# Kernel tuning notes

Measured on AMD Instinct MI355X. Metric: run time of the kernel, lower is better.

Reference implementation:

```python
import jax, jax.numpy as jnp
import numpy as np

N = 65536   # batch
G = 7       # grid
C = 2       # classes (cats vs dogs)
A = 3       # anchors


def _bce(p, t):
    return -(t * jnp.log(p) + (1.0 - t) * jnp.log(1.0 - p))


def _iou(a, b):
    # a, b: [..., 4] boxes in (cx, cy, w, h) format
    ax1, ay1 = a[..., 0] - a[..., 2] / 2, a[..., 1] - a[..., 3] / 2
    ax2, ay2 = a[..., 0] + a[..., 2] / 2, a[..., 1] + a[..., 3] / 2
    bx1, by1 = b[..., 0] - b[..., 2] / 2, b[..., 1] - b[..., 3] / 2
    bx2, by2 = b[..., 0] + b[..., 2] / 2, b[..., 1] + b[..., 3] / 2
    iw = jnp.clip(jnp.minimum(ax2, bx2) - jnp.maximum(ax1, bx1), 0.0)
    ih = jnp.clip(jnp.minimum(ay2, by2) - jnp.maximum(ay1, by1), 0.0)
    inter = iw * ih
    union = (ax2 - ax1) * (ay2 - ay1) + (bx2 - bx1) * (by2 - by1) - inter
    return inter / (union + 1e-9)


def setup_inputs():
    key = jax.random.key(0)
    k1, k2, k3, k4 = jax.random.split(key, 4)
    # probabilities / box params must lie strictly in (0,1) for BCE and log()
    bbox_ = jax.random.uniform(k1, (N, 15, G, G), dtype=jnp.float32, minval=0.01, maxval=0.99)
    bbox = jax.random.uniform(k2, (N, 5, G, G), dtype=jnp.float32, minval=0.01, maxval=0.99)
    cls_ = jax.random.normal(k3, (N, C), dtype=jnp.float32)
    cls = jax.random.randint(k4, (N,), 1, 3).astype(jnp.int64)  # labels in {1,2}
    return {"bbox_": bbox_, "cls_": cls_, "bbox": bbox, "cls": cls}


def reference(bbox_, cls_, bbox, cls):
    n = bbox.shape[0]
    bidx = jnp.arange(n)

    # classification: CrossEntropyLoss (mean) with labels cls-1
    logp = jax.nn.log_softmax(cls_, axis=-1)
    ce = -jnp.mean(jnp.take_along_axis(logp, (cls - 1)[:, None], axis=1))

    # argmax cell of GT objectness map per sample
    probs = bbox[:, 0]                       # [N,7,7]
    m = jnp.argmax(probs.reshape(n, -1), axis=1)
    i, j = m // G, m % G                     # [N], [N]

    cell_gt = bbox[bidx, :, i, j]            # [N,5]
    cell_pr = bbox_[bidx, :, i, j].reshape(n, A, 5)  # [N,3,5]

    jf = j.astype(bbox.dtype)
    if_ = i.astype(bbox.dtype)

    # target box in global coords
    tgt = jnp.stack([(cell_gt[:, 1] + jf) / G, (cell_gt[:, 2] + if_) / G,
                     cell_gt[:, 3], cell_gt[:, 4]], axis=-1)          # [N,4]
    # anchor boxes in global coords
    anc = jnp.stack([(cell_pr[:, :, 1] + jf[:, None]) / G,
                     (cell_pr[:, :, 2] + if_[:, None]) / G,
                     cell_pr[:, :, 3], cell_pr[:, :, 4]], axis=-1)    # [N,3,4]

    best = jnp.argmax(_iou(anc, tgt[:, None, :]), axis=1)             # [N]

    # target objectness maps: best anchor channel gets GT prob map
    target_prob = jnp.zeros((n, A, G, G), dtype=bbox.dtype)
    target_prob = target_prob.at[bidx, best].set(probs)

    # coordinate BCE (sum) + size L1-of-logs (sum) at the matched cell/anchor
    best_box = cell_pr[bidx, best]           # [N,5]
    coord = jnp.sum(_bce(best_box[:, 1:3], cell_gt[:, 1:3]))
    size = jnp.sum(jnp.abs(jnp.log(best_box[:, 3:5]) - jnp.log(cell_gt[:, 3:5])))

    # per-anchor objectness BCE (mean over N*49 each)
    prob_loss = (jnp.mean(_bce(bbox_[:, 0], target_prob[:, 0]))
                 + jnp.mean(_bce(bbox_[:, 5], target_prob[:, 1]))
                 + jnp.mean(_bce(bbox_[:, 10], target_prob[:, 2])))

    return ce + coord + size + prob_loss
```

## Files before the change

### kernel.cpp

```cpp
#include <hip/hip_runtime.h>
#include <math.h>


static constexpr int GG  = 49;
static constexpr int PRD = 15 * GG;
static constexpr int GTD = 5  * GG;
static constexpr int GOF = 768;
static constexpr int LPW = 1024;

__global__ void zero_kernel(float* out) { if (threadIdx.x == 0) out[0] = 0.0f; }

__global__ __launch_bounds__(256) void loss_kernel(
    const float* __restrict__ pr_all,
    const float* __restrict__ cls_logits,
    const float* __restrict__ gt_all,
    const int*   __restrict__ cls_lbl,
    float* __restrict__ out, int N)
{
    const int lane  = threadIdx.x & 63;
    const int wslot = threadIdx.x >> 6;
    const int wid   = blockIdx.x * (blockDim.x >> 6) + wslot;
    const int nwaves = gridDim.x * (blockDim.x >> 6);
    const float invG   = 1.0f / 7.0f;
    const float invN   = 1.0f / (float)N;
    const float invN49 = 1.0f / ((float)N * 49.0f);

    __shared__ float L[4][LPW];
    float* __restrict__ Lw = L[wslot];

    float acc = 0.0f;

    for (int n = wid; n < N; n += nwaves) {
        const float* pr = pr_all + (size_t)n * PRD;
        const float* gt = gt_all + (size_t)n * GTD;

        const float x0 = __builtin_nontemporal_load(cls_logits + 2 * n);
        const float x1 = __builtin_nontemporal_load(cls_logits + 2 * n + 1);
        const int   cl = __builtin_nontemporal_load(cls_lbl + n);

        float p[12];
        #pragma unroll
        for (int k = 0; k < 12; ++k) {
            int d = lane + 64 * k;
            if (d > PRD - 1) d = PRD - 1;
            p[k] = __builtin_nontemporal_load(pr + d);
        }
        float g[4];
        #pragma unroll
        for (int k = 0; k < 4; ++k) {
            int d = lane + 64 * k;
            if (d > GTD - 1) d = GTD - 1;
            g[k] = __builtin_nontemporal_load(gt + d);
        }

        #pragma unroll
        for (int k = 0; k < 12; ++k) {
            int d = lane + 64 * k;
            if (d > PRD - 1) d = PRD - 1;
            Lw[d] = p[k];
        }
        #pragma unroll
        for (int k = 0; k < 4; ++k) {
            int d = lane + 64 * k;
            if (d > GTD - 1) d = GTD - 1;
            Lw[GOF + d] = g[k];
        }
        asm volatile("s_waitcnt lgkmcnt(0)" ::: "memory");

        const float t = (lane < GG) ? g[0] : -1.0f;
        float v = t;
        #pragma unroll
        for (int off = 32; off; off >>= 1) v = fmaxf(v, __shfl_xor(v, off));
        const unsigned long long eq = __ballot(t == v);
        const int m  = __ffsll(eq) - 1;
        const int mi = m / 7, mj = m - mi * 7;
        const float jf = (float)mj, if_ = (float)mi;

        const float g1v = Lw[GOF +  49 + m];
        const float g2v = Lw[GOF +  98 + m];
        const float g3v = Lw[GOF + 147 + m];
        const float g4v = Lw[GOF + 196 + m];

        const float tx  = (g1v + jf) * invG;
        const float ty  = (g2v + if_) * invG;
        const float tx1 = tx - g3v * 0.5f, tx2 = tx + g3v * 0.5f;
        const float ty1 = ty - g4v * 0.5f, ty2 = ty + g4v * 0.5f;
        const float tarea = (tx2 - tx1) * (ty2 - ty1);

        int best = 0; float bestIoU = -1.0f;
        float px = 0.f, py = 0.f, pw = 0.f, ph = 0.f;
        #pragma unroll
        for (int a = 0; a < 3; a++) {
            const float c1 = Lw[(5 * a + 1) * GG + m];
            const float c2 = Lw[(5 * a + 2) * GG + m];
            const float c3 = Lw[(5 * a + 3) * GG + m];
            const float c4 = Lw[(5 * a + 4) * GG + m];
            const float ax  = (c1 + jf) * invG;
            const float ay  = (c2 + if_) * invG;
            const float ax1 = ax - c3 * 0.5f, ax2 = ax + c3 * 0.5f;
            const float ay1 = ay - c4 * 0.5f, ay2 = ay + c4 * 0.5f;
            float iw = fminf(ax2, tx2) - fmaxf(ax1, tx1); iw = fmaxf(iw, 0.0f);
            float ih = fminf(ay2, ty2) - fmaxf(ay1, ty1); ih = fmaxf(ih, 0.0f);
            const float inter = iw * ih;
            const float uni   = (ax2 - ax1) * (ay2 - ay1) + tarea - inter;
            const float iou   = inter / (uni + 1e-9f);
            if (iou > bestIoU) { bestIoU = iou; best = a; px = c1; py = c2; pw = c3; ph = c4; }
        }

        float s = 0.0f;
        if (lane < GG) {
            const float p0 = p[0];
            const float p1 = Lw[5 * GG  + lane];
            const float p2 = Lw[10 * GG + lane];
            const float l0 = __logf(1.0f - p0);
            const float l1 = __logf(1.0f - p1);
            const float l2 = __logf(1.0f - p2);
            s = -(l0 + l1 + l2);
            const float pbv  = (best == 0) ? p0 : (best == 1) ? p1 : p2;
            const float l1pb = (best == 0) ? l0 : (best == 1) ? l1 : l2;
            s -= t * (__logf(pbv) - l1pb);
        }
        acc += s * invN49;

        const float s0  = (lane < 4) ? ((lane < 2) ? px : py)
                                     : ((lane < 6) ? pw : ph);
        const float s1  = (lane < 4) ? (1.0f - s0)
                                     : ((lane < 6) ? g3v : g4v);
        const float la  = (lane & 1) ? s1 : s0;
        const float Lv  = __logf(la);
        const float Lx  = __shfl_xor(Lv, 1);
        float contrib = 0.0f;
        if (lane < 4) {
            const float w = (lane < 2) ? ((lane & 1) ? 1.0f - g1v : g1v)
                                       : ((lane & 1) ? 1.0f - g2v : g2v);
            contrib = -w * Lv;
        } else if (lane == 4 || lane == 6) {
            contrib = fabsf(Lv - Lx);
        }
        acc += contrib;

        if (lane == 5) {
            const float mx  = fmaxf(x0, x1);
            const float lse = mx + __logf(1.0f + __expf(-fabsf(x0 - x1)));
            const float lp  = ((cl == 1) ? x0 : x1) - lse;
            acc -= lp * invN;
        }
    }

    #pragma unroll
    for (int off = 32; off; off >>= 1) acc += __shfl_xor(acc, off);
    __shared__ float wsum[4];
    if (lane == 0) wsum[wslot] = acc;
    __syncthreads();
    if (threadIdx.x == 0) {
        atomicAdd(out, wsum[0] + wsum[1] + wsum[2] + wsum[3]);
    }
}

extern "C" void kernel_launch(void* const* d_in, const int* in_sizes, int n_in,
                              void* d_out, int out_size, void* d_ws, size_t ws_size,
                              hipStream_t stream) {
    const float* bbox_p = (const float*)d_in[0];
    const float* cls_p  = (const float*)d_in[1];
    const float* bbox_g = (const float*)d_in[2];
    const int*   cls_l  = (const int*)d_in[3];
    float* out = (float*)d_out;
    const int N = in_sizes[3];

    hipLaunchKernelGGL(zero_kernel, dim3(1), dim3(64), 0, stream, out);
    hipLaunchKernelGGL(loss_kernel, dim3(2048), dim3(256), 0, stream,
                       bbox_p, cls_p, bbox_g, cls_l, out, N);
}
```

Before: 296.7 us.

## Replace LDS staging with register readlane and shuffle-based gathers

New measurement: 301.7 us. About the same (+1.7%).

```diff
diff --git a/kernel.cpp b/kernel.cpp
--- a/kernel.cpp
+++ b/kernel.cpp
@@ -5,10 +5,12 @@
 static constexpr int GG  = 49;
 static constexpr int PRD = 15 * GG;
 static constexpr int GTD = 5  * GG;
-static constexpr int GOF = 768;
-static constexpr int LPW = 1024;
 
 __global__ void zero_kernel(float* out) { if (threadIdx.x == 0) out[0] = 0.0f; }
+
+__device__ __forceinline__ float rdl(float x, int l) {
+    return __int_as_float(__builtin_amdgcn_readlane(__float_as_int(x), l & 63));
+}
 
 __global__ __launch_bounds__(256) void loss_kernel(
     const float* __restrict__ pr_all,
@@ -24,9 +26,6 @@
     const float invG   = 1.0f / 7.0f;
     const float invN   = 1.0f / (float)N;
     const float invN49 = 1.0f / ((float)N * 49.0f);
-
-    __shared__ float L[4][LPW];
-    float* __restrict__ Lw = L[wslot];
 
     float acc = 0.0f;
 
@@ -53,20 +52,6 @@
             g[k] = __builtin_nontemporal_load(gt + d);
         }
 
-        #pragma unroll
-        for (int k = 0; k < 12; ++k) {
-            int d = lane + 64 * k;
-            if (d > PRD - 1) d = PRD - 1;
-            Lw[d] = p[k];
-        }
-        #pragma unroll
-        for (int k = 0; k < 4; ++k) {
-            int d = lane + 64 * k;
-            if (d > GTD - 1) d = GTD - 1;
-            Lw[GOF + d] = g[k];
-        }
-        asm volatile("s_waitcnt lgkmcnt(0)" ::: "memory");
-
         const float t = (lane < GG) ? g[0] : -1.0f;
         float v = t;
         #pragma unroll
@@ -76,10 +61,11 @@
         const int mi = m / 7, mj = m - mi * 7;
         const float jf = (float)mj, if_ = (float)mi;
 
-        const float g1v = Lw[GOF +  49 + m];
-        const float g2v = Lw[GOF +  98 + m];
-        const float g3v = Lw[GOF + 147 + m];
-        const float g4v = Lw[GOF + 196 + m];
+        const int d1 = 49 + m, d2 = 98 + m, d3 = 147 + m, d4 = 196 + m;
+        const float g1v = (d1 < 64)  ? rdl(g[0], d1) : rdl(g[1], d1);
+        const float g2v = (d2 < 128) ? rdl(g[1], d2) : rdl(g[2], d2);
+        const float g3v = (d3 < 192) ? rdl(g[2], d3) : rdl(g[3], d3);
+        const float g4v = rdl(g[3], d4);
 
         const float tx  = (g1v + jf) * invG;
         const float ty  = (g2v + if_) * invG;
@@ -91,35 +77,49 @@
         float px = 0.f, py = 0.f, pw = 0.f, ph = 0.f;
         #pragma unroll
         for (int a = 0; a < 3; a++) {
-            const float c1 = Lw[(5 * a + 1) * GG + m];
-            const float c2 = Lw[(5 * a + 2) * GG + m];
-            const float c3 = Lw[(5 * a + 3) * GG + m];
-            const float c4 = Lw[(5 * a + 4) * GG + m];
-            const float ax  = (c1 + jf) * invG;
-            const float ay  = (c2 + if_) * invG;
-            const float ax1 = ax - c3 * 0.5f, ax2 = ax + c3 * 0.5f;
-            const float ay1 = ay - c4 * 0.5f, ay2 = ay + c4 * 0.5f;
+            float c[4];
+            #pragma unroll
+            for (int cc = 0; cc < 4; ++cc) {
+                const int S  = (5 * a + 1 + cc) * GG;
+                const int k0 = S >> 6;
+                const int k1 = (S + GG - 1) >> 6;
+                const int d  = S + m;
+                c[cc] = (k0 == k1) ? rdl(p[k0], d)
+                      : (((d >> 6) == k0) ? rdl(p[k0], d) : rdl(p[k1], d));
+            }
+            const float ax  = (c[0] + jf) * invG;
+            const float ay  = (c[1] + if_) * invG;
+            const float ax1 = ax - c[2] * 0.5f, ax2 = ax + c[2] * 0.5f;
+            const float ay1 = ay - c[3] * 0.5f, ay2 = ay + c[3] * 0.5f;
             float iw = fminf(ax2, tx2) - fmaxf(ax1, tx1); iw = fmaxf(iw, 0.0f);
             float ih = fminf(ay2, ty2) - fmaxf(ay1, ty1); ih = fmaxf(ih, 0.0f);
             const float inter = iw * ih;
             const float uni   = (ax2 - ax1) * (ay2 - ay1) + tarea - inter;
             const float iou   = inter / (uni + 1e-9f);
-            if (iou > bestIoU) { bestIoU = iou; best = a; px = c1; py = c2; pw = c3; ph = c4; }
+            if (iou > bestIoU) { bestIoU = iou; best = a;
+                                 px = c[0]; py = c[1]; pw = c[2]; ph = c[3]; }
         }
 
-        float s = 0.0f;
-        if (lane < GG) {
-            const float p0 = p[0];
-            const float p1 = Lw[5 * GG  + lane];
-            const float p2 = Lw[10 * GG + lane];
-            const float l0 = __logf(1.0f - p0);
-            const float l1 = __logf(1.0f - p1);
-            const float l2 = __logf(1.0f - p2);
-            s = -(l0 + l1 + l2);
-            const float pbv  = (best == 0) ? p0 : (best == 1) ? p1 : p2;
-            const float l1pb = (best == 0) ? l0 : (best == 1) ? l1 : l2;
-            s -= t * (__logf(pbv) - l1pb);
-        }
+        const float l0 = (lane < 49)  ? __logf(1.0f - p[0]) : 0.0f;
+        const float l3 = (lane >= 53) ? __logf(1.0f - p[3]) : 0.0f;
+        const float l4 = (lane < 38)  ? __logf(1.0f - p[4]) : 0.0f;
+        const float l7 = (lane >= 42) ? __logf(1.0f - p[7]) : 0.0f;
+        const float l8 = (lane < 27)  ? __logf(1.0f - p[8]) : 0.0f;
+        float s = -(l0 + l3 + l4 + l7 + l8);
+
+        const int  rot  = (best == 0) ? 0 : (best == 1) ? 11 : 22;
+        const float trot = best ? __shfl(t, (lane + rot) & 63) : t;
+        bool  act; float pbin, lb1;
+        if (best == 0)      { act = (lane < 49);
+                              pbin = p[0]; lb1 = l0; }
+        else if (best == 1) { act = (lane >= 53) || (lane < 38);
+                              pbin = (lane >= 53) ? p[3] : p[4];
+                              lb1  = (lane >= 53) ? l3   : l4; }
+        else                { act = (lane >= 42) || (lane < 27);
+                              pbin = (lane >= 42) ? p[7] : p[8];
+                              lb1  = (lane >= 42) ? l7   : l8; }
+        const float lpb = __logf(act ? pbin : 1.0f);
+        s -= act ? trot * (lpb - lb1) : 0.0f;
         acc += s * invN49;
 
         const float s0  = (lane < 4) ? ((lane < 2) ? px : py)
```
